# Kernel tuning notes

Measured on AMD Instinct MI355X. Metric: run time of the kernel, lower is better.

Reference implementation:

```python
import jax, jax.numpy as jnp
import numpy as np
import math

B, S, D, H = 2, 2048, 1024, 16
DH = D // H


def setup_inputs() -> dict:
    key = jax.random.key(0)
    ks = jax.random.split(key, 10)
    scale = 1.0 / math.sqrt(D)
    inp = {
        "x": jax.random.normal(ks[0], (B, S, D), dtype=jnp.float32),
        "valid_nums": jax.random.randint(ks[1], (B,), 1, S + 1, dtype=jnp.int32),
        "Wq": jax.random.normal(ks[2], (D, D), dtype=jnp.float32) * scale,
        "bq": jnp.zeros((D,), dtype=jnp.float32),
        "Wk": jax.random.normal(ks[3], (D, D), dtype=jnp.float32) * scale,
        "bk": jnp.zeros((D,), dtype=jnp.float32),
        "Wv": jax.random.normal(ks[4], (D, D), dtype=jnp.float32) * scale,
        "bv": jnp.zeros((D,), dtype=jnp.float32),
        "Wo": jax.random.normal(ks[5], (D, D), dtype=jnp.float32) * scale,
        "bo": jnp.zeros((D,), dtype=jnp.float32),
    }
    return inp


def _split_heads(t):
    # (B, S, D) -> (B, H, S, DH)
    return t.reshape(B, S, H, DH).transpose(0, 2, 1, 3)


def reference(x, valid_nums, Wq, bq, Wk, bk, Wv, bv, Wo, bo):
    q = _split_heads(x @ Wq + bq)
    k = _split_heads(x @ Wk + bk)
    v = _split_heads(x @ Wv + bv)
    scores = jnp.einsum("bhqd,bhkd->bhqk", q, k) / math.sqrt(DH)  # (B,H,S,S)
    # length mask over keys: key j valid iff j < valid_nums[b]
    key_mask = jnp.arange(S)[None, :] < valid_nums[:, None]        # (B,S)
    scores = jnp.where(key_mask[:, None, None, :], scores, -jnp.inf)
    attn = jax.nn.softmax(scores, axis=-1)
    out = jnp.einsum("bhqk,bhkd->bhqd", attn, v)                   # (B,H,S,DH)
    out = out.transpose(0, 2, 1, 3).reshape(B, S, D)
    return out @ Wo + bo
```

## Files before the change

### kernel.cpp

```cpp
#include <hip/hip_runtime.h>
#include <hip/hip_bf16.h>
#include <math.h>

static constexpr int Bb = 2, Ss = 2048, Dd = 1024, Hh = 16, DHh = 64;
static constexpr int Mm = Bb * Ss;
static constexpr int Kk = Dd;

typedef __attribute__((ext_vector_type(8))) short bf16x8;
typedef __attribute__((ext_vector_type(4))) float f32x4;
typedef unsigned short us;

__device__ inline short f2b(float f) {
    __hip_bfloat16 h = __float2bfloat16(f);
    return *reinterpret_cast<short*>(&h);
}
__device__ inline float b2f(us u) {
    __hip_bfloat16 h = *reinterpret_cast<__hip_bfloat16*>(&u);
    return __bfloat162float(h);
}
__device__ inline unsigned pk2(float lo, float hi) {
    return ((unsigned)(us)f2b(hi) << 16) | (unsigned)(us)f2b(lo);
}
__device__ inline float ex2(float x) {
    return __builtin_amdgcn_exp2f(x);
}

__device__ inline void gload16(us* lds, const us* g) {
    __builtin_amdgcn_global_load_lds(
        (const __attribute__((address_space(1))) void*)g,
        (__attribute__((address_space(3))) void*)lds,
        16, 0, 0);
}

__global__ __launch_bounds__(256)
void xconv_kernel(const float* __restrict__ x, us* __restrict__ xb)
{
    const size_t i = ((size_t)blockIdx.x * 256 + threadIdx.x) * 8;
    float4 a = *(const float4*)(x + i);
    float4 b = *(const float4*)(x + i + 4);
    bf16x8 t;
    t[0] = f2b(a.x); t[1] = f2b(a.y); t[2] = f2b(a.z); t[3] = f2b(a.w);
    t[4] = f2b(b.x); t[5] = f2b(b.y); t[6] = f2b(b.z); t[7] = f2b(b.w);
    *(bf16x8*)(xb + i) = t;
}

__global__ __launch_bounds__(256)
void wtrans_kernel(const float* __restrict__ Wq, const float* __restrict__ Wk,
                   const float* __restrict__ Wv, const float* __restrict__ Wo,
                   us* __restrict__ Wt, us* __restrict__ Woth, us* __restrict__ Wotl)
{
    __shared__ float T[64][65];
    const int z = blockIdx.z;
    const float* W = (z == 0) ? Wq : (z == 1) ? Wk : (z == 2) ? Wv : Wo;
    const int split = (z == 3);
    us* dh = split ? Woth : (Wt + (size_t)z * Dd * Kk);
    us* dl = Wotl;

    const int n0 = blockIdx.x * 64, k0 = blockIdx.y * 64;
    const int tid = threadIdx.x;
    const int r = tid >> 2, c0 = (tid & 3) * 16;
#pragma unroll
    for (int j = 0; j < 4; ++j) {
        float4 v = *(const float4*)(W + (size_t)(k0 + r) * Dd + n0 + c0 + 4 * j);
        T[r][c0 + 4 * j + 0] = v.x;
        T[r][c0 + 4 * j + 1] = v.y;
        T[r][c0 + 4 * j + 2] = v.z;
        T[r][c0 + 4 * j + 3] = v.w;
    }
    __syncthreads();
    us hi[16], lo[16];
#pragma unroll
    for (int j = 0; j < 16; ++j) {
        float v = T[c0 + j][r];
        us h = (us)f2b(v);
        hi[j] = h;
        if (split) lo[j] = (us)f2b(v - b2f(h));
    }
    *(bf16x8*)&dh[(size_t)(n0 + r) * Kk + k0 + c0]     = *(bf16x8*)&hi[0];
    *(bf16x8*)&dh[(size_t)(n0 + r) * Kk + k0 + c0 + 8] = *(bf16x8*)&hi[8];
    if (split) {
        *(bf16x8*)&dl[(size_t)(n0 + r) * Kk + k0 + c0]     = *(bf16x8*)&lo[0];
        *(bf16x8*)&dl[(size_t)(n0 + r) * Kk + k0 + c0 + 8] = *(bf16x8*)&lo[8];
    }
}

__global__ __launch_bounds__(256)
void gemm_qkv_kernel(const us* __restrict__ xb, const us* __restrict__ Wt,
                     const float* __restrict__ bq, const float* __restrict__ bk,
                     const float* __restrict__ bv, us* __restrict__ QKV)
{
    __shared__ us As[128 * 64];
    __shared__ us Bs[128 * 64];
    const int tid = threadIdx.x;
    const int wave = tid >> 6, lane = tid & 63;
    const int wr = wave >> 1, wc = wave & 1;
    const int lg = lane >> 4, ll = lane & 15;
    const int col0 = blockIdx.x * 128;
    const int row0 = blockIdx.y * 128;

    f32x4 acc[4][4];
#pragma unroll
    for (int mt = 0; mt < 4; ++mt)
#pragma unroll
        for (int nt = 0; nt < 4; ++nt)
#pragma unroll
            for (int r = 0; r < 4; ++r) acc[mt][nt][r] = 0.f;

    const us* Ag = xb + (size_t)(row0 + wave * 32 + (lane >> 3)) * Kk + (lane & 7) * 8;
    const us* Bg = Wt + (size_t)(col0 + wave * 32 + (lane >> 3)) * Kk + (lane & 7) * 8;
    us* Ad = &As[(wave * 4) * 512];
    us* Bd = &Bs[(wave * 4) * 512];

    for (int k0 = 0; k0 < Kk; k0 += 64) {
        __syncthreads();
#pragma unroll
        for (int i = 0; i < 4; ++i) {
            gload16(Ad + i * 512, Ag + (size_t)(i * 8) * Kk + k0);
            gload16(Bd + i * 512, Bg + (size_t)(i * 8) * Kk + k0);
        }
        __syncthreads();
#pragma unroll
        for (int ks = 0; ks < 2; ++ks) {
            bf16x8 af[4], bfr[4];
#pragma unroll
            for (int mt = 0; mt < 4; ++mt)
                af[mt] = *(const bf16x8*)&As[(wr * 64 + mt * 16 + ll) * 64 + ks * 32 + lg * 8];
#pragma unroll
            for (int nt = 0; nt < 4; ++nt)
                bfr[nt] = *(const bf16x8*)&Bs[(wc * 64 + nt * 16 + ll) * 64 + ks * 32 + lg * 8];
#pragma unroll
            for (int mt = 0; mt < 4; ++mt)
#pragma unroll
                for (int nt = 0; nt < 4; ++nt)
                    acc[mt][nt] = __builtin_amdgcn_mfma_f32_16x16x32_bf16(af[mt], bfr[nt], acc[mt][nt], 0, 0, 0);
        }
    }

    const int z = col0 >> 10;
    const int c0 = col0 & 1023;
    const float* bias = (z == 0) ? bq : (z == 1) ? bk : bv;
    const float osc = (z == 0) ? 0.125f * 1.44269504f : 1.0f;
    us* outz = QKV + (size_t)z * Mm * Dd;

    if (z == 2) {
#pragma unroll
        for (int mt = 0; mt < 4; ++mt)
#pragma unroll
            for (int nt = 0; nt < 4; ++nt) {
                int row = row0 + wr * 64 + mt * 16 + lg * 4;
                int col = c0 + wc * 64 + nt * 16 + ll;
                int b_ = row >> 11, s_ = row & 2047;
                float bv_ = bias[col];
                union { us u[4]; uint2 d2; } pk;
#pragma unroll
                for (int r = 0; r < 4; ++r) pk.u[r] = (us)f2b(acc[mt][nt][r] + bv_);
                *(uint2*)&outz[((size_t)(b_ * Hh * DHh) + col) * Ss + s_] = pk.d2;
            }
    } else {
#pragma unroll
        for (int mt = 0; mt < 4; ++mt)
#pragma unroll
            for (int nt = 0; nt < 4; ++nt)
#pragma unroll
                for (int r = 0; r < 4; ++r) {
                    int row = row0 + wr * 64 + mt * 16 + lg * 4 + r;
                    int col = c0 + wc * 64 + nt * 16 + ll;
                    float v = (acc[mt][nt][r] + bias[col]) * osc;
                    int b_ = row >> 11, s_ = row & 2047, h_ = col >> 6, d_ = col & 63;
                    outz[(((size_t)(b_ * Hh + h_)) * Ss + s_) * DHh + d_] = (us)f2b(v);
                }
    }
}

__global__ __launch_bounds__(256)
void gemm_final_kernel(const us* __restrict__ Oh, const us* __restrict__ Ol,
                       const us* __restrict__ Wth, const us* __restrict__ Wtl,
                       const float* __restrict__ bo, float* __restrict__ out)
{
    __shared__ us AhS[128 * 64];
    __shared__ us AlS[128 * 64];
    __shared__ us BhS[64 * 64];
    __shared__ us BlS[64 * 64];
    const int tid = threadIdx.x;
    const int wave = tid >> 6, lane = tid & 63;
    const int wr = wave >> 1, wc = wave & 1;
    const int lg = lane >> 4, ll = lane & 15;
    const int col0 = blockIdx.x * 64;
    const int row0 = blockIdx.y * 128;

    f32x4 acc[4][2];
#pragma unroll
    for (int mt = 0; mt < 4; ++mt)
#pragma unroll
        for (int nt = 0; nt < 2; ++nt)
#pragma unroll
            for (int r = 0; r < 4; ++r) acc[mt][nt][r] = 0.f;

    const size_t aoff = (size_t)(row0 + wave * 32 + (lane >> 3)) * Kk + (lane & 7) * 8;
    const size_t boff = (size_t)(col0 + wave * 16 + (lane >> 3)) * Kk + (lane & 7) * 8;
    const us* Ahg = Oh + aoff;
    const us* Alg = Ol + aoff;
    const us* Bhg = Wth + boff;
    const us* Blg = Wtl + boff;
    us* AhD = &AhS[(wave * 4) * 512];
    us* AlD = &AlS[(wave * 4) * 512];
    us* BhD = &BhS[(wave * 2) * 512];
    us* BlD = &BlS[(wave * 2) * 512];

    for (int k0 = 0; k0 < Kk; k0 += 64) {
        __syncthreads();
#pragma unroll
        for (int i = 0; i < 4; ++i) {
            gload16(AhD + i * 512, Ahg + (size_t)(i * 8) * Kk + k0);
            gload16(AlD + i * 512, Alg + (size_t)(i * 8) * Kk + k0);
        }
#pragma unroll
        for (int j = 0; j < 2; ++j) {
            gload16(BhD + j * 512, Bhg + (size_t)(j * 8) * Kk + k0);
            gload16(BlD + j * 512, Blg + (size_t)(j * 8) * Kk + k0);
        }
        __syncthreads();
#pragma unroll
        for (int ks = 0; ks < 2; ++ks) {
            bf16x8 ah[4], al[4], bh[2], bl[2];
#pragma unroll
            for (int mt = 0; mt < 4; ++mt) {
                ah[mt] = *(const bf16x8*)&AhS[(wr * 64 + mt * 16 + ll) * 64 + ks * 32 + lg * 8];
                al[mt] = *(const bf16x8*)&AlS[(wr * 64 + mt * 16 + ll) * 64 + ks * 32 + lg * 8];
            }
#pragma unroll
            for (int nt = 0; nt < 2; ++nt) {
                bh[nt] = *(const bf16x8*)&BhS[(wc * 32 + nt * 16 + ll) * 64 + ks * 32 + lg * 8];
                bl[nt] = *(const bf16x8*)&BlS[(wc * 32 + nt * 16 + ll) * 64 + ks * 32 + lg * 8];
            }
#pragma unroll
            for (int mt = 0; mt < 4; ++mt)
#pragma unroll
                for (int nt = 0; nt < 2; ++nt) {
                    acc[mt][nt] = __builtin_amdgcn_mfma_f32_16x16x32_bf16(ah[mt], bh[nt], acc[mt][nt], 0, 0, 0);
                    acc[mt][nt] = __builtin_amdgcn_mfma_f32_16x16x32_bf16(al[mt], bh[nt], acc[mt][nt], 0, 0, 0);
                    acc[mt][nt] = __builtin_amdgcn_mfma_f32_16x16x32_bf16(ah[mt], bl[nt], acc[mt][nt], 0, 0, 0);
                }
        }
    }

#pragma unroll
    for (int mt = 0; mt < 4; ++mt)
#pragma unroll
        for (int nt = 0; nt < 2; ++nt)
#pragma unroll
            for (int r = 0; r < 4; ++r) {
                int row = row0 + wr * 64 + mt * 16 + lg * 4 + r;
                int col = col0 + wc * 32 + nt * 16 + ll;
                out[(size_t)row * Dd + col] = acc[mt][nt][r] + bo[col];
            }
}

__global__ __launch_bounds__(512)
void attn_mfma_kernel(const us* __restrict__ Q, const us* __restrict__ K,
                      const us* __restrict__ Vt_g, const int* __restrict__ valid_nums,
                      us* __restrict__ Oh, us* __restrict__ Ol)
{
    const int id  = blockIdx.x;
    const int xcd = id & 7, grp = id >> 3;
    const int bh  = (grp >> 4) * 8 + xcd;
    const int qb  = grp & 15;
    const int b   = bh >> 4, h = bh & 15;
    const int q0  = qb * 128;

    const int tid  = threadIdx.x;
    const int wave = tid >> 6;
    const int lane = tid & 63;
    const int lg = lane >> 4;
    const int ll = lane & 15;

    const int nv = valid_nums[b];
    const int ntiles = (nv + 63) >> 6;

    const us* Qb = Q    + (size_t)bh * Ss * DHh;
    const us* Kb = K    + (size_t)bh * Ss * DHh;
    const us* Vb = Vt_g + (size_t)bh * DHh * Ss;

    __shared__ us Ks[64][68];
    __shared__ us Vs[64][68];

    bf16x8 qa[2];
    {
        const us* qrow = Qb + (size_t)(q0 + wave * 16 + ll) * DHh;
        qa[0] = *(const bf16x8*)(qrow + lg * 8);
        qa[1] = *(const bf16x8*)(qrow + 32 + lg * 8);
    }

    union { unsigned w[4]; bf16x8 v; } ones_u;
#pragma unroll
    for (int i = 0; i < 4; ++i) ones_u.w[i] = 0x3F803F80u;
    const bf16x8 vones = ones_u.v;

    f32x4 o[4], o4;
#pragma unroll
    for (int nt = 0; nt < 4; ++nt) { o[nt][0]=0.f; o[nt][1]=0.f; o[nt][2]=0.f; o[nt][3]=0.f; }
    o4[0]=0.f; o4[1]=0.f; o4[2]=0.f; o4[3]=0.f;
    float mq = -INFINITY;

    const int srow = tid >> 3;
    const int scol = (tid & 7) * 8;

    bf16x8 kreg = *(const bf16x8*)(Kb + (size_t)srow * DHh + scol);
    bf16x8 vreg = *(const bf16x8*)(Vb + (size_t)srow * Ss + scol);

    for (int kt = 0; kt < ntiles; ++kt) {
        const int k0 = kt * 64;
        __syncthreads();
        *(bf16x8*)&Ks[srow][scol] = kreg;
        *(bf16x8*)&Vs[srow][scol] = vreg;
        __syncthreads();
        if (kt + 1 < ntiles) {
            kreg = *(const bf16x8*)(Kb + (size_t)(k0 + 64 + srow) * DHh + scol);
            vreg = *(const bf16x8*)(Vb + (size_t)srow * Ss + k0 + 64 + scol);
        }

        f32x4 s[4];
#pragma unroll
        for (int nt = 0; nt < 4; ++nt) { s[nt][0]=0.f; s[nt][1]=0.f; s[nt][2]=0.f; s[nt][3]=0.f; }
#pragma unroll
        for (int ks = 0; ks < 2; ++ks) {
#pragma unroll
            for (int nt = 0; nt < 4; ++nt) {
                bf16x8 kf = *(const bf16x8*)&Ks[nt * 16 + ll][ks * 32 + lg * 8];
                s[nt] = __builtin_amdgcn_mfma_f32_16x16x32_bf16(kf, qa[ks], s[nt], 0, 0, 0);
            }
        }

        float p[4][4];
        float mx;
        if (k0 + 64 <= nv) {
#pragma unroll
            for (int nt = 0; nt < 4; ++nt)
#pragma unroll
                for (int r = 0; r < 4; ++r) p[nt][r] = s[nt][r];
            mx = fmaxf(fmaxf(fmaxf(p[0][0], p[0][1]), fmaxf(p[0][2], p[0][3])),
                       fmaxf(fmaxf(p[1][0], p[1][1]), fmaxf(p[1][2], p[1][3])));
            mx = fmaxf(mx,
                 fmaxf(fmaxf(fmaxf(p[2][0], p[2][1]), fmaxf(p[2][2], p[2][3])),
                       fmaxf(fmaxf(p[3][0], p[3][1]), fmaxf(p[3][2], p[3][3]))));
        } else {
            mx = -INFINITY;
#pragma unroll
            for (int nt = 0; nt < 4; ++nt)
#pragma unroll
                for (int r = 0; r < 4; ++r) {
                    int key = k0 + nt * 16 + lg * 4 + r;
                    float v = (key < nv) ? s[nt][r] : -INFINITY;
                    p[nt][r] = v;
                    mx = fmaxf(mx, v);
                }
        }
        mx = fmaxf(mx, __shfl_xor(mx, 16));
        mx = fmaxf(mx, __shfl_xor(mx, 32));

        const bool rescale = !__all(mx <= mq + 11.5f);
        if (rescale) {
            float mn = fmaxf(mq, mx);
            float corr = ex2(mq - mn);
            mq = mn;
            float corr4[4];
#pragma unroll
            for (int r = 0; r < 4; ++r) corr4[r] = __shfl(corr, lg * 16 + lg * 4 + r);
#pragma unroll
            for (int nt = 0; nt < 4; ++nt)
#pragma unroll
                for (int r = 0; r < 4; ++r) o[nt][r] *= corr4[r];
#pragma unroll
            for (int r = 0; r < 4; ++r) o4[r] *= corr4[r];
        }

#pragma unroll
        for (int nt = 0; nt < 4; ++nt)
#pragma unroll
            for (int r = 0; r < 4; ++r) p[nt][r] = ex2(p[nt][r] - mq);

        unsigned dw[4][2];
#pragma unroll
        for (int nt = 0; nt < 4; ++nt) {
            dw[nt][0] = pk2(p[nt][0], p[nt][1]);
            dw[nt][1] = pk2(p[nt][2], p[nt][3]);
        }

        const int sA = ((2 * lg) & 3) * 16 + ll;
        const int sB = ((2 * lg + 1) & 3) * 16 + ll;
        const bool hi = (lg & 2);
#pragma unroll
        for (int ks = 0; ks < 2; ++ks) {
            unsigned a0 = (unsigned)__shfl((int)dw[2 * ks][0],     sA);
            unsigned a1 = (unsigned)__shfl((int)dw[2 * ks][1],     sA);
            unsigned a2 = (unsigned)__shfl((int)dw[2 * ks][0],     sB);
            unsigned a3 = (unsigned)__shfl((int)dw[2 * ks][1],     sB);
            unsigned b0 = (unsigned)__shfl((int)dw[2 * ks + 1][0], sA);
            unsigned b1 = (unsigned)__shfl((int)dw[2 * ks + 1][1], sA);
            unsigned b2 = (unsigned)__shfl((int)dw[2 * ks + 1][0], sB);
            unsigned b3 = (unsigned)__shfl((int)dw[2 * ks + 1][1], sB);
            union { unsigned w[4]; bf16x8 v; } pa;
            pa.w[0] = hi ? b0 : a0;
            pa.w[1] = hi ? b1 : a1;
            pa.w[2] = hi ? b2 : a2;
            pa.w[3] = hi ? b3 : a3;
#pragma unroll
            for (int nt = 0; nt < 4; ++nt) {
                bf16x8 vb = *(const bf16x8*)&Vs[nt * 16 + ll][ks * 32 + lg * 8];
                o[nt] = __builtin_amdgcn_mfma_f32_16x16x32_bf16(pa.v, vb, o[nt], 0, 0, 0);
            }
            o4 = __builtin_amdgcn_mfma_f32_16x16x32_bf16(pa.v, vones, o4, 0, 0, 0);
        }
    }

#pragma unroll
    for (int r = 0; r < 4; ++r) {
        int row = q0 + wave * 16 + lg * 4 + r;
        float linv = 1.f / o4[r];
#pragma unroll
        for (int nt = 0; nt < 4; ++nt) {
            float val = o[nt][r] * linv;
            us uh = (us)f2b(val);
            float rem = val - b2f(uh);
            size_t base = ((size_t)b * Ss + row) * Dd + h * DHh + nt * 16 + ll;
            Oh[base] = uh;
            Ol[base] = (us)f2b(rem);
        }
    }
}

extern "C" void kernel_launch(void* const* d_in, const int* in_sizes, int n_in,
                              void* d_out, int out_size, void* d_ws, size_t ws_size,
                              hipStream_t stream) {
    const float* x     = (const float*)d_in[0];
    const int*   valid = (const int*)d_in[1];
    const float* Wq = (const float*)d_in[2];
    const float* bq = (const float*)d_in[3];
    const float* Wk = (const float*)d_in[4];
    const float* bk = (const float*)d_in[5];
    const float* Wv = (const float*)d_in[6];
    const float* bv = (const float*)d_in[7];
    const float* Wo = (const float*)d_in[8];
    const float* bo = (const float*)d_in[9];

    const size_t per = (size_t)Mm * Dd;
    const size_t wsz = (size_t)Dd * Kk;
    us* wsp  = (us*)d_ws;
    us* QKV  = wsp;
    us* Wt   = QKV + 3 * per;
    us* OhB  = Wt + 3 * wsz;
    us* OlB  = OhB + per;
    us* Woth = OlB + per;
    us* Wotl = Woth + wsz;
    us* xb   = Wotl + wsz;

    xconv_kernel<<<(Mm * Kk) / (256 * 8), 256, 0, stream>>>(x, xb);

    wtrans_kernel<<<dim3(Dd / 64, Kk / 64, 4), 256, 0, stream>>>(
        Wq, Wk, Wv, Wo, Wt, Woth, Wotl);

    gemm_qkv_kernel<<<dim3(3 * Dd / 128, Mm / 128), 256, 0, stream>>>(
        xb, Wt, bq, bk, bv, QKV);

    attn_mfma_kernel<<<(Ss / 128) * (Bb * Hh), 512, 0, stream>>>(
        QKV, QKV + per, QKV + 2 * per, valid, OhB, OlB);

    gemm_final_kernel<<<dim3(Dd / 64, Mm / 128), 256, 0, stream>>>(
        OhB, OlB, Woth, Wotl, bo, (float*)d_out);
}
```

Measured before the change: 145.8 us.

## Double-buffer QKV GEMM LDS and widen attention key tiles to 128

The QKV GEMM now uses two LDS buffers and issues the next K-slice's global-to-LDS loads before computing on the current one, leaving one barrier per iteration instead of two. The attention kernel processes 128 keys per tile instead of 64, which halves the number of barriers and softmax max/rescale rounds. It also pads the LDS arrays differently and raises wave priority around the MFMA sections with s_setprio. The costs are more LDS and register use per block, which may reduce occupancy, and more wasted masked work on the last tile when the valid length is short.

```diff
diff --git a/kernel.cpp b/kernel.cpp
--- a/kernel.cpp
+++ b/kernel.cpp
@@ -89,8 +89,8 @@
                      const float* __restrict__ bq, const float* __restrict__ bk,
                      const float* __restrict__ bv, us* __restrict__ QKV)
 {
-    __shared__ us As[128 * 64];
-    __shared__ us Bs[128 * 64];
+    __shared__ us As[2][128 * 64];
+    __shared__ us Bs[2][128 * 64];
     const int tid = threadIdx.x;
     const int wave = tid >> 6, lane = tid & 63;
     const int wr = wave >> 1, wc = wave & 1;
@@ -108,32 +108,41 @@
 
     const us* Ag = xb + (size_t)(row0 + wave * 32 + (lane >> 3)) * Kk + (lane & 7) * 8;
     const us* Bg = Wt + (size_t)(col0 + wave * 32 + (lane >> 3)) * Kk + (lane & 7) * 8;
-    us* Ad = &As[(wave * 4) * 512];
-    us* Bd = &Bs[(wave * 4) * 512];
-
-    for (int k0 = 0; k0 < Kk; k0 += 64) {
-        __syncthreads();
-#pragma unroll
-        for (int i = 0; i < 4; ++i) {
-            gload16(Ad + i * 512, Ag + (size_t)(i * 8) * Kk + k0);
-            gload16(Bd + i * 512, Bg + (size_t)(i * 8) * Kk + k0);
-        }
-        __syncthreads();
+    const int ldsb = (wave * 4) * 512;
+
+#pragma unroll
+    for (int i = 0; i < 4; ++i) {
+        gload16(&As[0][ldsb + i * 512], Ag + (size_t)(i * 8) * Kk);
+        gload16(&Bs[0][ldsb + i * 512], Bg + (size_t)(i * 8) * Kk);
+    }
+    __syncthreads();
+
+    for (int it = 0; it < 16; ++it) {
+        const int sb = it & 1;
+        if (it < 15) {
+            const int kn = (it + 1) * 64;
+#pragma unroll
+            for (int i = 0; i < 4; ++i) {
+                gload16(&As[sb ^ 1][ldsb + i * 512], Ag + (size_t)(i * 8) * Kk + kn);
+                gload16(&Bs[sb ^ 1][ldsb + i * 512], Bg + (size_t)(i * 8) * Kk + kn);
+            }
+        }
 #pragma unroll
         for (int ks = 0; ks < 2; ++ks) {
             bf16x8 af[4], bfr[4];
 #pragma unroll
             for (int mt = 0; mt < 4; ++mt)
-                af[mt] = *(const bf16x8*)&As[(wr * 64 + mt * 16 + ll) * 64 + ks * 32 + lg * 8];
+                af[mt] = *(const bf16x8*)&As[sb][(wr * 64 + mt * 16 + ll) * 64 + ks * 32 + lg * 8];
 #pragma unroll
             for (int nt = 0; nt < 4; ++nt)
-                bfr[nt] = *(const bf16x8*)&Bs[(wc * 64 + nt * 16 + ll) * 64 + ks * 32 + lg * 8];
+                bfr[nt] = *(const bf16x8*)&Bs[sb][(wc * 64 + nt * 16 + ll) * 64 + ks * 32 + lg * 8];
 #pragma unroll
             for (int mt = 0; mt < 4; ++mt)
 #pragma unroll
                 for (int nt = 0; nt < 4; ++nt)
                     acc[mt][nt] = __builtin_amdgcn_mfma_f32_16x16x32_bf16(af[mt], bfr[nt], acc[mt][nt], 0, 0, 0);
         }
+        __syncthreads();
     }
 
     const int z = col0 >> 10;
@@ -275,14 +284,14 @@
     const int ll = lane & 15;
 
     const int nv = valid_nums[b];
-    const int ntiles = (nv + 63) >> 6;
+    const int ntiles = (nv + 127) >> 7;
 
     const us* Qb = Q    + (size_t)bh * Ss * DHh;
     const us* Kb = K    + (size_t)bh * Ss * DHh;
     const us* Vb = Vt_g + (size_t)bh * DHh * Ss;
 
-    __shared__ us Ks[64][68];
-    __shared__ us Vs[64][68];
+    __shared__ us Ks[128][72];
+    __shared__ us Vs[64][136];
 
     bf16x8 qa[2];
     {
@@ -302,56 +311,64 @@
     o4[0]=0.f; o4[1]=0.f; o4[2]=0.f; o4[3]=0.f;
     float mq = -INFINITY;
 
-    const int srow = tid >> 3;
+    const int krow = tid >> 3;
     const int scol = (tid & 7) * 8;
 
-    bf16x8 kreg = *(const bf16x8*)(Kb + (size_t)srow * DHh + scol);
-    bf16x8 vreg = *(const bf16x8*)(Vb + (size_t)srow * Ss + scol);
+    bf16x8 kr0 = *(const bf16x8*)(Kb + (size_t)krow * DHh + scol);
+    bf16x8 kr1 = *(const bf16x8*)(Kb + (size_t)(64 + krow) * DHh + scol);
+    bf16x8 vr0 = *(const bf16x8*)(Vb + (size_t)krow * Ss + scol);
+    bf16x8 vr1 = *(const bf16x8*)(Vb + (size_t)krow * Ss + 64 + scol);
+
+    const int l0 = (2 * (lg & 1)) * 16 + ll;
+    const int l1 = l0 + 16;
+    const bool hi = (lg & 2);
 
     for (int kt = 0; kt < ntiles; ++kt) {
-        const int k0 = kt * 64;
+        const int k0 = kt << 7;
         __syncthreads();
-        *(bf16x8*)&Ks[srow][scol] = kreg;
-        *(bf16x8*)&Vs[srow][scol] = vreg;
+        *(bf16x8*)&Ks[krow][scol]      = kr0;
+        *(bf16x8*)&Ks[krow + 64][scol] = kr1;
+        *(bf16x8*)&Vs[krow][scol]      = vr0;
+        *(bf16x8*)&Vs[krow][64 + scol] = vr1;
         __syncthreads();
         if (kt + 1 < ntiles) {
-            kreg = *(const bf16x8*)(Kb + (size_t)(k0 + 64 + srow) * DHh + scol);
-            vreg = *(const bf16x8*)(Vb + (size_t)srow * Ss + k0 + 64 + scol);
-        }
-
-        f32x4 s[4];
-#pragma unroll
-        for (int nt = 0; nt < 4; ++nt) { s[nt][0]=0.f; s[nt][1]=0.f; s[nt][2]=0.f; s[nt][3]=0.f; }
+            const int kn = k0 + 128;
+            kr0 = *(const bf16x8*)(Kb + (size_t)(kn + krow) * DHh + scol);
+            kr1 = *(const bf16x8*)(Kb + (size_t)(kn + 64 + krow) * DHh + scol);
+            vr0 = *(const bf16x8*)(Vb + (size_t)krow * Ss + kn + scol);
+            vr1 = *(const bf16x8*)(Vb + (size_t)krow * Ss + kn + 64 + scol);
+        }
+
+        f32x4 s[8];
+#pragma unroll
+        for (int nt = 0; nt < 8; ++nt) { s[nt][0]=0.f; s[nt][1]=0.f; s[nt][2]=0.f; s[nt][3]=0.f; }
+        __builtin_amdgcn_s_setprio(1);
 #pragma unroll
         for (int ks = 0; ks < 2; ++ks) {
 #pragma unroll
-            for (int nt = 0; nt < 4; ++nt) {
+            for (int nt = 0; nt < 8; ++nt) {
                 bf16x8 kf = *(const bf16x8*)&Ks[nt * 16 + ll][ks * 32 + lg * 8];
                 s[nt] = __builtin_amdgcn_mfma_f32_16x16x32_bf16(kf, qa[ks], s[nt], 0, 0, 0);
             }
         }
-
-        float p[4][4];
+        __builtin_amdgcn_s_setprio(0);
+
         float mx;
-        if (k0 + 64 <= nv) {
-#pragma unroll
-            for (int nt = 0; nt < 4; ++nt)
-#pragma unroll
-                for (int r = 0; r < 4; ++r) p[nt][r] = s[nt][r];
-            mx = fmaxf(fmaxf(fmaxf(p[0][0], p[0][1]), fmaxf(p[0][2], p[0][3])),
-                       fmaxf(fmaxf(p[1][0], p[1][1]), fmaxf(p[1][2], p[1][3])));
-            mx = fmaxf(mx,
-                 fmaxf(fmaxf(fmaxf(p[2][0], p[2][1]), fmaxf(p[2][2], p[2][3])),
-                       fmaxf(fmaxf(p[3][0], p[3][1]), fmaxf(p[3][2], p[3][3]))));
+        if (k0 + 128 <= nv) {
+            mx = -INFINITY;
+#pragma unroll
+            for (int nt = 0; nt < 8; ++nt)
+#pragma unroll
+                for (int r = 0; r < 4; ++r) mx = fmaxf(mx, s[nt][r]);
         } else {
             mx = -INFINITY;
 #pragma unroll
-            for (int nt = 0; nt < 4; ++nt)
+            for (int nt = 0; nt < 8; ++nt)
 #pragma unroll
                 for (int r = 0; r < 4; ++r) {
                     int key = k0 + nt * 16 + lg * 4 + r;
                     float v = (key < nv) ? s[nt][r] : -INFINITY;
-                    p[nt][r] = v;
+                    s[nt][r] = v;
                     mx = fmaxf(mx, v);
                 }
         }
@@ -375,41 +392,38 @@
         }
 
 #pragma unroll
-        for (int nt = 0; nt < 4; ++nt)
-#pragma unroll
-            for (int r = 0; r < 4; ++r) p[nt][r] = ex2(p[nt][r] - mq);
-
-        unsigned dw[4][2];
-#pragma unroll
-        for (int nt = 0; nt < 4; ++nt) {
-            dw[nt][0] = pk2(p[nt][0], p[nt][1]);
-            dw[nt][1] = pk2(p[nt][2], p[nt][3]);
-        }
-
-        const int sA = ((2 * lg) & 3) * 16 + ll;
-        const int sB = ((2 * lg + 1) & 3) * 16 + ll;
-        const bool hi = (lg & 2);
-#pragma unroll
-        for (int ks = 0; ks < 2; ++ks) {
-            unsigned a0 = (unsigned)__shfl((int)dw[2 * ks][0],     sA);
-            unsigned a1 = (unsigned)__shfl((int)dw[2 * ks][1],     sA);
-            unsigned a2 = (unsigned)__shfl((int)dw[2 * ks][0],     sB);
-            unsigned a3 = (unsigned)__shfl((int)dw[2 * ks][1],     sB);
-            unsigned b0 = (unsigned)__shfl((int)dw[2 * ks + 1][0], sA);
-            unsigned b1 = (unsigned)__shfl((int)dw[2 * ks + 1][1], sA);
-            unsigned b2 = (unsigned)__shfl((int)dw[2 * ks + 1][0], sB);
-            unsigned b3 = (unsigned)__shfl((int)dw[2 * ks + 1][1], sB);
+        for (int g = 0; g < 4; ++g) {
+            float pA[4], pB[4];
+#pragma unroll
+            for (int r = 0; r < 4; ++r) {
+                pA[r] = ex2(s[2 * g][r] - mq);
+                pB[r] = ex2(s[2 * g + 1][r] - mq);
+            }
+            unsigned dA0 = pk2(pA[0], pA[1]), dA1 = pk2(pA[2], pA[3]);
+            unsigned dB0 = pk2(pB[0], pB[1]), dB1 = pk2(pB[2], pB[3]);
+
+            unsigned a0 = (unsigned)__shfl((int)dA0, l0);
+            unsigned a1 = (unsigned)__shfl((int)dA1, l0);
+            unsigned a2 = (unsigned)__shfl((int)dA0, l1);
+            unsigned a3 = (unsigned)__shfl((int)dA1, l1);
+            unsigned b0 = (unsigned)__shfl((int)dB0, l0);
+            unsigned b1 = (unsigned)__shfl((int)dB1, l0);
+            unsigned b2 = (unsigned)__shfl((int)dB0, l1);
+            unsigned b3 = (unsigned)__shfl((int)dB1, l1);
             union { unsigned w[4]; bf16x8 v; } pa;
             pa.w[0] = hi ? b0 : a0;
             pa.w[1] = hi ? b1 : a1;
             pa.w[2] = hi ? b2 : a2;
             pa.w[3] = hi ? b3 : a3;
+
+            __builtin_amdgcn_s_setprio(1);
 #pragma unroll
             for (int nt = 0; nt < 4; ++nt) {
-                bf16x8 vb = *(const bf16x8*)&Vs[nt * 16 + ll][ks * 32 + lg * 8];
+                bf16x8 vb = *(const bf16x8*)&Vs[nt * 16 + ll][g * 32 + lg * 8];
                 o[nt] = __builtin_amdgcn_mfma_f32_16x16x32_bf16(pa.v, vb, o[nt], 0, 0, 0);
             }
             o4 = __builtin_amdgcn_mfma_f32_16x16x32_bf16(pa.v, vones, o4, 0, 0, 0);
+            __builtin_amdgcn_s_setprio(0);
         }
     }
 
```

After: 155.6 us. 6.8% more time.
